# Kernel tuning notes

Hardware: AMD Instinct MI355X
Metric: run time of the kernel (lower is better)

Reference implementation:

```python
import jax, jax.numpy as jnp
import numpy as np

HEAD = 16
CONV = 32
DEF = CONV * 8  # 256
SCALE = jnp.float32(np.sqrt(DEF))  # sqrt(256) = 16


def setup_inputs() -> dict:
    key = jax.random.key(0)
    k1, k2, k3, k4 = jax.random.split(key, 4)
    bsz = 4096
    drug = jax.random.normal(k1, (bsz, DEF), dtype=jnp.float32)
    protein = jax.random.normal(k2, (bsz, DEF), dtype=jnp.float32)
    # Linear(256 -> 4096) weights, stored [in, out]; bias zeros
    W_d = jax.random.normal(k3, (DEF, DEF * HEAD), dtype=jnp.float32) * (1.0 / np.sqrt(DEF))
    b_d = jnp.zeros((DEF * HEAD,), dtype=jnp.float32)
    W_p = jax.random.normal(k4, (DEF, DEF * HEAD), dtype=jnp.float32) * (1.0 / np.sqrt(DEF))
    b_p = jnp.zeros((DEF * HEAD,), dtype=jnp.float32)
    return {"drug": drug, "protein": protein, "W_d": W_d, "b_d": b_d, "W_p": W_p, "b_p": b_p}


def reference(drug, protein, W_d, b_d, W_p, b_p):
    bsz = drug.shape[0]
    # ReLU(linear) then reshape: drug -> [b, 256, head]; protein -> [b, head, 256]
    drug_att = jax.nn.relu(drug @ W_d + b_d).reshape(bsz, DEF, HEAD)
    protein_att = jax.nn.relu(protein @ W_p + b_p).reshape(bsz, HEAD, DEF)
    # interaction map [b, 256, 256]
    imap = jnp.tanh(jnp.einsum('bdh,bhp->bdp', drug_att, protein_att) / SCALE)
    compound_atte = jnp.tanh(jnp.sum(imap, axis=2))  # [b, 256]
    protein_atte = jnp.tanh(jnp.sum(imap, axis=1))   # [b, 256]
    return (drug * compound_atte, protein * protein_atte)
```

## Files before the change

### kernel.cpp

```cpp
#include <hip/hip_runtime.h>
#include <stdint.h>

typedef unsigned short u16;
typedef u16   u16x4 __attribute__((ext_vector_type(4)));
typedef u16   u16x8 __attribute__((ext_vector_type(8)));
typedef short v8s   __attribute__((ext_vector_type(8)));
typedef float v4f   __attribute__((ext_vector_type(4)));
typedef float f4    __attribute__((ext_vector_type(4)));

#if __has_builtin(__builtin_amdgcn_exp2f)
#define EXP2F(x) __builtin_amdgcn_exp2f(x)
#else
#define EXP2F(x) exp2f(x)
#endif
#if __has_builtin(__builtin_amdgcn_rcpf)
#define RCPF(x) __builtin_amdgcn_rcpf(x)
#else
#define RCPF(x) (1.0f/(x))
#endif

__device__ __forceinline__ float b2f(u16 u) {
    unsigned int i = ((unsigned int)u) << 16;
    float f; __builtin_memcpy(&f, &i, 4); return f;
}
__device__ __forceinline__ u16 f2b(float f) {
    unsigned int x; __builtin_memcpy(&x, &f, 4);
    x += 0x7fffu + ((x >> 16) & 1u);
    return (u16)(x >> 16);
}
__device__ __forceinline__ float tanhp(float x) {
    float e = EXP2F(2.8853900817779268f * x);
    return 1.0f - 2.0f * RCPF(1.0f + e);
}
__device__ __forceinline__ void g2l16(const u16* g, u16* l) {
    __builtin_amdgcn_global_load_lds(
        (const __attribute__((address_space(1))) unsigned int*)g,
        (__attribute__((address_space(3))) unsigned int*)l, 16, 0, 0);
}

__global__ __launch_bounds__(256) void cvt_rows(
    const float* __restrict__ X0, const float* __restrict__ X1,
    u16* __restrict__ O0, u16* __restrict__ O1) {
    const float* X = blockIdx.z ? X1 : X0;
    u16*         O = blockIdx.z ? O1 : O0;
    size_t i = ((size_t)blockIdx.x * 256 + threadIdx.x) * 8;
    f4 a = *(const f4*)(X + i), b = *(const f4*)(X + i + 4);
    u16x8 r;
    r[0] = f2b(a[0]); r[1] = f2b(a[1]); r[2] = f2b(a[2]); r[3] = f2b(a[3]);
    r[4] = f2b(b[0]); r[5] = f2b(b[1]); r[6] = f2b(b[2]); r[7] = f2b(b[3]);
    *(u16x8*)(O + i) = r;
}

__global__ __launch_bounds__(256) void wtrans(
    const float* __restrict__ W0, const float* __restrict__ W1,
    u16* __restrict__ T0, u16* __restrict__ T1) {
    int z = blockIdx.z;
    const float* W = z ? W1 : W0;
    u16*         T = z ? T1 : T0;
    __shared__ u16 t[32][36];
    int k0 = blockIdx.x * 32, n0 = blockIdx.y * 32;
    int r = threadIdx.x >> 3, c = (threadIdx.x & 7) * 4;
    f4 v = *(const f4*)(W + (size_t)(k0 + r) * 4096 + n0 + c);
    t[r][c + 0] = f2b(v[0]); t[r][c + 1] = f2b(v[1]);
    t[r][c + 2] = f2b(v[2]); t[r][c + 3] = f2b(v[3]);
    __syncthreads();
    u16x4 o;
    o.x = t[c + 0][r]; o.y = t[c + 1][r]; o.z = t[c + 2][r]; o.w = t[c + 3][r];
    int n = n0 + r;
    int row = z ? ((n & 255) * 16 + (n >> 8)) : n;
    *(u16x4*)(T + (size_t)row * 256 + k0 + c) = o;
}

__global__ __launch_bounds__(256) void gemm_relu(
    const u16* __restrict__ A0, const u16* __restrict__ A1,
    const u16* __restrict__ B0, const u16* __restrict__ B1,
    const float* __restrict__ bias0, const float* __restrict__ bias1,
    u16* __restrict__ R0, u16* __restrict__ R1) {
    int z = blockIdx.z;
    const u16*   A    = z ? A1 : A0;
    const u16*   Bt   = z ? B1 : B0;
    const float* bias = z ? bias1 : bias0;
    u16*         R    = z ? R1 : R0;

    __shared__ __align__(16) u16 As[128 * 32];
    __shared__ __align__(16) u16 Bs[128 * 32];

    int tid  = threadIdx.x;
    int lane = tid & 63;
    int wave = tid >> 6;
    int m0 = blockIdx.x * 128, n0 = blockIdx.y * 128;
    int wm = (wave >> 1) * 64, wn = (wave & 1) * 64;

    v4f acc[4][4] = {};

    int f0 = tid, f1 = tid + 256;
    int r0 = f0 >> 2, c0 = (f0 & 3) * 8;
    int r1 = f1 >> 2, c1 = (f1 & 3) * 8;
    const u16* Ab = A  + (size_t)m0 * 256;
    const u16* Bb = Bt + (size_t)n0 * 256;
    int rsel = lane & 15, ksel = (lane >> 4) * 8;

    for (int kk = 0; kk < 256; kk += 32) {
        __syncthreads();
        g2l16(Ab + r0 * 256 + kk + c0, As + f0 * 8);
        g2l16(Ab + r1 * 256 + kk + c1, As + f1 * 8);
        g2l16(Bb + r0 * 256 + kk + c0, Bs + f0 * 8);
        g2l16(Bb + r1 * 256 + kk + c1, Bs + f1 * 8);
        __syncthreads();
        v8s af[4], bf[4];
#pragma unroll
        for (int mi = 0; mi < 4; mi++)
            af[mi] = *(const v8s*)(As + (wm + mi * 16 + rsel) * 32 + ksel);
#pragma unroll
        for (int ni = 0; ni < 4; ni++)
            bf[ni] = *(const v8s*)(Bs + (wn + ni * 16 + rsel) * 32 + ksel);
#pragma unroll
        for (int mi = 0; mi < 4; mi++)
#pragma unroll
            for (int ni = 0; ni < 4; ni++)
                acc[mi][ni] = __builtin_amdgcn_mfma_f32_16x16x32_bf16(af[mi], bf[ni], acc[mi][ni], 0, 0, 0);
    }

    int rb = (lane >> 4) * 4;
#pragma unroll
    for (int ni = 0; ni < 4; ni++) {
        int col = n0 + wn + ni * 16 + rsel;
        int bcol = z ? ((col & 15) * 256 + (col >> 4)) : col;
        float bv = bias[bcol];
#pragma unroll
        for (int mi = 0; mi < 4; mi++) {
#pragma unroll
            for (int r = 0; r < 4; r++) {
                int row = m0 + wm + mi * 16 + rb + r;
                R[(size_t)row * 4096 + col] = f2b(fmaxf(acc[mi][ni][r] + bv, 0.0f));
            }
        }
    }
}

__global__ __launch_bounds__(256, 4) void stage2(
    const u16* __restrict__ Rd, const u16* __restrict__ Rp,
    const float* __restrict__ drug, const float* __restrict__ protein,
    float* __restrict__ out, int bo) {
    int bl = blockIdx.x;
    int b  = bo + bl;
    __shared__ __align__(16) u16 Ad[4096];
    __shared__ __align__(16) u16 Bp[4096];
    __shared__ float rowq[256];
    __shared__ float colq[1024];

    int tid = threadIdx.x, lane = tid & 63, wave = tid >> 6;
    {
        const u16* rd = Rd + (size_t)bl * 4096;
        const u16* rp = Rp + (size_t)bl * 4096;
        g2l16(rd + tid * 8,         Ad + tid * 8);
        g2l16(rd + (tid + 256) * 8, Ad + (tid + 256) * 8);
        g2l16(rp + tid * 8,         Bp + tid * 8);
        g2l16(rp + (tid + 256) * 8, Bp + (tid + 256) * 8);
    }
    __syncthreads();

    int  mr = lane & 15;
    int  kg = lane >> 4;
    int  ko = (kg & 1) * 8;
    bool act = kg < 2;
    v8s zero8 = {};
    v4f czero = {};

    v8s af[4];
#pragma unroll
    for (int s = 0; s < 4; ++s) {
        v8s ld = *(const v8s*)(Ad + (wave * 64 + s * 16 + mr) * 16 + ko);
        af[s] = act ? ld : zero8;
    }

    v4f rsq[4] = {czero, czero, czero, czero};
    const float S2 = 0.18033688f;
#pragma unroll 2
    for (int ni = 0; ni < 16; ++ni) {
        v8s bf = *(const v8s*)(Bp + (ni * 16 + mr) * 16 + ko);
        v4f cq = czero;
#pragma unroll
        for (int s = 0; s < 4; ++s) {
            v4f c = __builtin_amdgcn_mfma_f32_16x16x32_bf16(af[s], bf, czero, 0, 0, 0);
            v4f q;
#pragma unroll
            for (int t = 0; t < 4; ++t)
                q[t] = RCPF(1.0f + EXP2F(c[t] * S2));
            rsq[s] += q;
            cq += q;
        }
        float cp = (cq[0] + cq[1]) + (cq[2] + cq[3]);
        cp += __shfl_xor(cp, 16);
        cp += __shfl_xor(cp, 32);
        if (lane < 16) colq[wave * 256 + ni * 16 + lane] = cp;
    }
#pragma unroll
    for (int s = 0; s < 4; ++s)
#pragma unroll
        for (int t = 0; t < 4; ++t) {
            float v = rsq[s][t];
            v += __shfl_xor(v, 1);
            v += __shfl_xor(v, 2);
            v += __shfl_xor(v, 4);
            v += __shfl_xor(v, 8);
            if (mr == 0) rowq[wave * 64 + s * 16 + kg * 4 + t] = v;
        }
    __syncthreads();
    float qc = colq[tid] + colq[256 + tid] + colq[512 + tid] + colq[768 + tid];
    float ca = tanhp(256.0f - 2.0f * rowq[tid]);
    float pa = tanhp(256.0f - 2.0f * qc);
    size_t o = (size_t)b * 256 + tid;
    out[o]           = drug[o]    * ca;
    out[1048576 + o] = protein[o] * pa;
}

__global__ __launch_bounds__(256) void fused_fallback(
    const float* __restrict__ drug, const float* __restrict__ protein,
    const float* __restrict__ Wd,   const float* __restrict__ bd,
    const float* __restrict__ Wp,   const float* __restrict__ bp,
    float* __restrict__ out)
{
    __shared__ __align__(16) u16 smem[73856];
    u16*   dRow = smem;
    u16*   pRow = smem + 2048;
    u16*   Ws   = smem + 4096;
    float* rowsum  = (float*)(smem + 4096);
    float* colpart = rowsum + 256;
    u16*   dAtt = smem + 8320;
    u16*   pAtt = smem + 41088;

    int tid = threadIdx.x, lane = tid & 63, wave = tid >> 6;
    int b0  = blockIdx.x * 8;
    int mr  = lane & 15;
    int kg  = lane >> 4;
    int ksel = kg * 8;

    {
        int row = tid >> 5, c = (tid & 31) * 8;
        const float* ps = drug + (size_t)(b0 + row) * 256 + c;
        const float* qs = protein + (size_t)(b0 + row) * 256 + c;
        u16x8 r1, r2;
#pragma unroll
        for (int j = 0; j < 8; ++j) { r1[j] = f2b(ps[j]); r2[j] = f2b(qs[j]); }
        *(u16x8*)(dRow + row * 256 + c) = r1;
        *(u16x8*)(pRow + row * 256 + c) = r2;
    }

    int r0 = tid >> 4;
    int c0 = (tid & 15) * 8;
    for (int which = 0; which < 2; ++which) {
        const float* W      = which ? Wp   : Wd;
        const float* bias   = which ? bp   : bd;
        const u16*   rowbuf = which ? pRow : dRow;
        u16*         att    = which ? pAtt : dAtt;

        for (int n0 = 0; n0 < 4096; n0 += 128) {
            v4f acc0 = {}, acc1 = {};
            int wn = wave * 32;
            u16x8 pf0, pf1;
            {
                const float* p0 = W + (size_t)(r0) * 4096 + n0 + c0;
                const float* p1 = W + (size_t)(r0 + 16) * 4096 + n0 + c0;
#pragma unroll
                for (int j = 0; j < 8; ++j) { pf0[j] = f2b(p0[j]); pf1[j] = f2b(p1[j]); }
            }
            for (int k0 = 0; k0 < 256; k0 += 32) {
                __syncthreads();
                *(u16x4*)(Ws + r0 * 132 + c0)            = ((u16x4*)&pf0)[0];
                *(u16x4*)(Ws + r0 * 132 + c0 + 4)        = ((u16x4*)&pf0)[1];
                *(u16x4*)(Ws + (r0 + 16) * 132 + c0)     = ((u16x4*)&pf1)[0];
                *(u16x4*)(Ws + (r0 + 16) * 132 + c0 + 4) = ((u16x4*)&pf1)[1];
                __syncthreads();
                if (k0 + 32 < 256) {
                    const float* p0 = W + (size_t)(k0 + 32 + r0) * 4096 + n0 + c0;
                    const float* p1 = W + (size_t)(k0 + 32 + r0 + 16) * 4096 + n0 + c0;
#pragma unroll
                    for (int j = 0; j < 8; ++j) { pf0[j] = f2b(p0[j]); pf1[j] = f2b(p1[j]); }
                }
                v8s af = {};
                if (mr < 8) af = *(const v8s*)(rowbuf + mr * 256 + k0 + ksel);
                v8s bf0, bf1;
                int nA = wn + mr, nB = wn + 16 + mr;
#pragma unroll
                for (int j = 0; j < 8; ++j) {
                    bf0[j] = (short)Ws[(ksel + j) * 132 + nA];
                    bf1[j] = (short)Ws[(ksel + j) * 132 + nB];
                }
                acc0 = __builtin_amdgcn_mfma_f32_16x16x32_bf16(af, bf0, acc0, 0, 0, 0);
                acc1 = __builtin_amdgcn_mfma_f32_16x16x32_bf16(af, bf1, acc1, 0, 0, 0);
            }
            int colA = n0 + wn + mr, colB = colA + 16;
            float bvA = bias[colA], bvB = bias[colB];
#pragma unroll
            for (int t = 0; t < 4; ++t) {
                int row = kg * 4 + t;
                if (row < 8) {
                    u16 vA = f2b(fmaxf(acc0[t] + bvA, 0.0f));
                    u16 vB = f2b(fmaxf(acc1[t] + bvB, 0.0f));
                    if (which == 0) {
                        att[row * 4096 + colA] = vA;
                        att[row * 4096 + colB] = vB;
                    } else {
                        att[row * 4096 + (colA & 255) * 16 + (colA >> 8)] = vA;
                        att[row * 4096 + (colB & 255) * 16 + (colB >> 8)] = vB;
                    }
                }
            }
        }
    }
    __syncthreads();

    v8s zero8 = {};
    v4f czero = {};
    int  ko2  = (kg & 1) * 8;
    bool act2 = kg < 2;
    for (int r = 0; r < 8; ++r) {
        const u16* Ar = dAtt + r * 4096;
        const u16* Br = pAtt + r * 4096;
        v8s af2[4];
#pragma unroll
        for (int s = 0; s < 4; ++s) {
            int d = wave * 64 + s * 16 + mr;
            v8s ld = *(const v8s*)(Ar + d * 16 + ko2);
            af2[s] = act2 ? ld : zero8;
        }
        float rs[4][4] = {};
#pragma unroll
        for (int ni = 0; ni < 16; ++ni) {
            int p = ni * 16 + mr;
            v8s lb = *(const v8s*)(Br + p * 16 + ko2);
            v8s bf = act2 ? lb : zero8;
            float cp = 0.0f;
#pragma unroll
            for (int s = 0; s < 4; ++s) {
                v4f c = __builtin_amdgcn_mfma_f32_16x16x32_bf16(af2[s], bf, czero, 0, 0, 0);
#pragma unroll
                for (int t = 0; t < 4; ++t) {
                    float v = tanhp(c[t] * 0.0625f);
                    rs[s][t] += v;
                    cp += v;
                }
            }
            cp += __shfl_xor(cp, 16);
            cp += __shfl_xor(cp, 32);
            if (lane < 16) colpart[wave * 256 + ni * 16 + lane] = cp;
        }
#pragma unroll
        for (int s = 0; s < 4; ++s)
#pragma unroll
            for (int t = 0; t < 4; ++t) {
                float v = rs[s][t];
                v += __shfl_xor(v, 1);
                v += __shfl_xor(v, 2);
                v += __shfl_xor(v, 4);
                v += __shfl_xor(v, 8);
                if (mr == 0) rowsum[wave * 64 + s * 16 + kg * 4 + t] = v;
            }
        __syncthreads();
        float cs = colpart[tid] + colpart[256 + tid] + colpart[512 + tid] + colpart[768 + tid];
        float ca = tanhp(rowsum[tid]);
        float pa = tanhp(cs);
        size_t o = (size_t)(b0 + r) * 256 + tid;
        out[o]           = drug[o]    * ca;
        out[1048576 + o] = protein[o] * pa;
        __syncthreads();
    }
}

extern "C" void kernel_launch(void* const* d_in, const int* in_sizes, int n_in,
                              void* d_out, int out_size, void* d_ws, size_t ws_size,
                              hipStream_t stream) {
    (void)in_sizes; (void)n_in; (void)out_size;
    const float* drug    = (const float*)d_in[0];
    const float* protein = (const float*)d_in[1];
    const float* Wd      = (const float*)d_in[2];
    const float* bd      = (const float*)d_in[3];
    const float* Wp      = (const float*)d_in[4];
    const float* bp      = (const float*)d_in[5];
    float* out = (float*)d_out;

    const size_t FIXED = (size_t)8 * 1024 * 1024;
    size_t avail = (ws_size > FIXED) ? ws_size - FIXED : 0;
    int chunk = (int)(avail / (2 * 4096 * sizeof(u16)));
    chunk = (chunk / 128) * 128;
    if (chunk > 4096) chunk = 4096;

    if (chunk >= 128) {
        u16* ws  = (u16*)d_ws;
        u16* Ad  = ws;
        u16* Ap  = Ad + (1u << 20);
        u16* Wtd = Ap + (1u << 20);
        u16* Wtp = Wtd + (1u << 20);
        u16* Rd  = Wtp + (1u << 20);
        u16* Rp  = Rd + (size_t)chunk * 4096;

        cvt_rows<<<dim3(512, 1, 2), 256, 0, stream>>>(drug, protein, Ad, Ap);
        wtrans  <<<dim3(8, 128, 2), 256, 0, stream>>>(Wd, Wp, Wtd, Wtp);
        for (int bo = 0; bo < 4096; bo += chunk) {
            int rows = (4096 - bo < chunk) ? (4096 - bo) : chunk;
            gemm_relu<<<dim3(rows / 128, 32, 2), 256, 0, stream>>>(
                Ad + (size_t)bo * 256, Ap + (size_t)bo * 256,
                Wtd, Wtp, bd, bp, Rd, Rp);
            stage2<<<dim3(rows), 256, 0, stream>>>(Rd, Rp, drug, protein, out, bo);
        }
    } else {
        fused_fallback<<<dim3(512), 256, 0, stream>>>(drug, protein, Wd, bd, Wp, bp, out);
    }
}
```

Before: 175.3 us.

## Widen GEMM K-tile with XOR-swizzled LDS, fold scale into epilogue, raise stage2 occupancy

The ReLU GEMM now loads 64-wide K slices per barrier pair with an XOR swizzle on LDS columns, which halves the number of synchronisations and is meant to avoid bank conflicts on fragment reads. The tanh scale factor is split across both operands as a per-element multiply in the GEMM epilogue, so stage2 no longer multiplies every MFMA output by a constant. Stage2 reuses the operand LDS buffer for its row and column partial sums and raises the occupancy hint to 8 blocks, at the cost of an extra barrier. Scaling before the bf16 rounding changes rounding slightly.

```diff
diff --git a/kernel.cpp b/kernel.cpp
--- a/kernel.cpp
+++ b/kernel.cpp
@@ -37,6 +37,8 @@
         (const __attribute__((address_space(1))) unsigned int*)g,
         (__attribute__((address_space(3))) unsigned int*)l, 16, 0, 0);
 }
+
+#define RSCALE 0.42466090f
 
 __global__ __launch_bounds__(256) void cvt_rows(
     const float* __restrict__ X0, const float* __restrict__ X1,
@@ -82,8 +84,8 @@
     const float* bias = z ? bias1 : bias0;
     u16*         R    = z ? R1 : R0;
 
-    __shared__ __align__(16) u16 As[128 * 32];
-    __shared__ __align__(16) u16 Bs[128 * 32];
+    __shared__ __align__(16) u16 As[128 * 64];
+    __shared__ __align__(16) u16 Bs[128 * 64];
 
     int tid  = threadIdx.x;
     int lane = tid & 63;
@@ -93,35 +95,43 @@
 
     v4f acc[4][4] = {};
 
-    int f0 = tid, f1 = tid + 256;
-    int r0 = f0 >> 2, c0 = (f0 & 3) * 8;
-    int r1 = f1 >> 2, c1 = (f1 & 3) * 8;
     const u16* Ab = A  + (size_t)m0 * 256;
     const u16* Bb = Bt + (size_t)n0 * 256;
-    int rsel = lane & 15, ksel = (lane >> 4) * 8;
-
-    for (int kk = 0; kk < 256; kk += 32) {
+    int rsel = lane & 15, kg = lane >> 4;
+
+    for (int kk = 0; kk < 256; kk += 64) {
         __syncthreads();
-        g2l16(Ab + r0 * 256 + kk + c0, As + f0 * 8);
-        g2l16(Ab + r1 * 256 + kk + c1, As + f1 * 8);
-        g2l16(Bb + r0 * 256 + kk + c0, Bs + f0 * 8);
-        g2l16(Bb + r1 * 256 + kk + c1, Bs + f1 * 8);
+#pragma unroll
+        for (int j = 0; j < 4; ++j) {
+            int f = tid + j * 256;
+            int r = f >> 3, cc = f & 7;
+            int gc = (cc ^ (r & 7)) * 8;
+            g2l16(Ab + (size_t)r * 256 + kk + gc, As + f * 8);
+            g2l16(Bb + (size_t)r * 256 + kk + gc, Bs + f * 8);
+        }
         __syncthreads();
-        v8s af[4], bf[4];
-#pragma unroll
-        for (int mi = 0; mi < 4; mi++)
-            af[mi] = *(const v8s*)(As + (wm + mi * 16 + rsel) * 32 + ksel);
-#pragma unroll
-        for (int ni = 0; ni < 4; ni++)
-            bf[ni] = *(const v8s*)(Bs + (wn + ni * 16 + rsel) * 32 + ksel);
-#pragma unroll
-        for (int mi = 0; mi < 4; mi++)
-#pragma unroll
-            for (int ni = 0; ni < 4; ni++)
-                acc[mi][ni] = __builtin_amdgcn_mfma_f32_16x16x32_bf16(af[mi], bf[ni], acc[mi][ni], 0, 0, 0);
-    }
-
-    int rb = (lane >> 4) * 4;
+#pragma unroll
+        for (int h = 0; h < 2; ++h) {
+            v8s af[4], bf[4];
+#pragma unroll
+            for (int mi = 0; mi < 4; mi++) {
+                int row = wm + mi * 16 + rsel;
+                af[mi] = *(const v8s*)(As + row * 64 + (((h * 4 + kg) ^ (row & 7)) * 8));
+            }
+#pragma unroll
+            for (int ni = 0; ni < 4; ni++) {
+                int row = wn + ni * 16 + rsel;
+                bf[ni] = *(const v8s*)(Bs + row * 64 + (((h * 4 + kg) ^ (row & 7)) * 8));
+            }
+#pragma unroll
+            for (int mi = 0; mi < 4; mi++)
+#pragma unroll
+                for (int ni = 0; ni < 4; ni++)
+                    acc[mi][ni] = __builtin_amdgcn_mfma_f32_16x16x32_bf16(af[mi], bf[ni], acc[mi][ni], 0, 0, 0);
+        }
+    }
+
+    int rb = kg * 4;
 #pragma unroll
     for (int ni = 0; ni < 4; ni++) {
         int col = n0 + wn + ni * 16 + rsel;
@@ -132,13 +142,13 @@
 #pragma unroll
             for (int r = 0; r < 4; r++) {
                 int row = m0 + wm + mi * 16 + rb + r;
-                R[(size_t)row * 4096 + col] = f2b(fmaxf(acc[mi][ni][r] + bv, 0.0f));
-            }
-        }
-    }
-}
-
-__global__ __launch_bounds__(256, 4) void stage2(
+                R[(size_t)row * 4096 + col] = f2b(fmaxf(acc[mi][ni][r] + bv, 0.0f) * RSCALE);
+            }
+        }
+    }
+}
+
+__global__ __launch_bounds__(256, 8) void stage2(
     const u16* __restrict__ Rd, const u16* __restrict__ Rp,
     const float* __restrict__ drug, const float* __restrict__ protein,
     float* __restrict__ out, int bo) {
@@ -146,8 +156,8 @@
     int b  = bo + bl;
     __shared__ __align__(16) u16 Ad[4096];
     __shared__ __align__(16) u16 Bp[4096];
-    __shared__ float rowq[256];
-    __shared__ float colq[1024];
+    float* rowq = (float*)Ad;
+    float* colq = rowq + 256;
 
     int tid = threadIdx.x, lane = tid & 63, wave = tid >> 6;
     {
@@ -173,9 +183,9 @@
         v8s ld = *(const v8s*)(Ad + (wave * 64 + s * 16 + mr) * 16 + ko);
         af[s] = act ? ld : zero8;
     }
+    __syncthreads();
 
     v4f rsq[4] = {czero, czero, czero, czero};
-    const float S2 = 0.18033688f;
 #pragma unroll 2
     for (int ni = 0; ni < 16; ++ni) {
         v8s bf = *(const v8s*)(Bp + (ni * 16 + mr) * 16 + ko);
@@ -186,7 +196,7 @@
             v4f q;
 #pragma unroll
             for (int t = 0; t < 4; ++t)
-                q[t] = RCPF(1.0f + EXP2F(c[t] * S2));
+                q[t] = RCPF(1.0f + EXP2F(c[t]));
             rsq[s] += q;
             cq += q;
         }
```

Result: slower. 229.6 us (+30.9%).
